# Kernel optimization log

Hardware: AMD Instinct MI355X
Metric: run time of the kernel (lower is better)

Reference implementation:

```python
import jax, jax.numpy as jnp
import numpy as np

MARGIN = 0.2  # TripletMarginLoss margin and TripletMarginMiner margin


def setup_inputs() -> dict:
    key = jax.random.key(0)
    k1, k2 = jax.random.split(key)
    embeddings = jax.random.normal(k1, (384, 256), dtype=jnp.float32)
    labels = jax.random.randint(k2, (384,), 0, 32)
    return {"embeddings": embeddings, "labels": labels}


def _pairwise_l2(e):
    # Euclidean distance matrix with sqrt-safe gradient at zero.
    sq = jnp.sum(e * e, axis=1)
    d2 = jnp.maximum(sq[:, None] + sq[None, :] - 2.0 * (e @ e.T), 0.0)
    pos = d2 > 0.0
    return jnp.sqrt(jnp.where(pos, d2, 1.0)) * pos


def reference(embeddings, labels):
    # pytorch-metric-learning LpDistance defaults: normalize_embeddings=True, p=2
    e = embeddings / jnp.maximum(
        jnp.linalg.norm(embeddings, axis=1, keepdims=True), 1e-12
    )
    D = _pairwise_l2(e)  # [B, B]
    n = D.shape[0]

    same = labels[:, None] == labels[None, :]
    eye = jnp.eye(n, dtype=bool)
    pos_mask = same & ~eye   # valid (anchor, positive) pairs
    neg_mask = ~same         # valid (anchor, negative) pairs

    ap = D[:, :, None]       # dist(anchor, positive), broadcast over negative
    an = D[:, None, :]       # dist(anchor, negative), broadcast over positive
    tm = an - ap             # miner's triplet_margin (is_inverted=False)

    valid = pos_mask[:, :, None] & neg_mask[:, None, :]     # [B, B, B]
    # semihard miner: 0 < an - ap <= margin
    semihard = valid & (tm > 0.0) & (tm <= MARGIN)

    # TripletMarginLoss per-triplet loss: relu(ap - an + margin) = relu(margin - tm)
    losses = jnp.where(semihard, jnp.maximum(MARGIN - tm, 0.0), 0.0)

    # AvgNonZeroReducer: mean over strictly-positive losses (0 if none)
    nz = jnp.sum(losses > 0.0)
    total = jnp.sum(losses)
    return jnp.where(nz > 0, total / jnp.maximum(nz, 1).astype(total.dtype), 0.0)
```

## Files before the change

kernel.cpp:

```cpp
#include <hip/hip_runtime.h>

#define N    384
#define DIM  256
#define MARGIN_F 0.2f


__global__ __launch_bounds__(DIM) void normalize_kernel(
    const float* __restrict__ emb, float* __restrict__ eT,
    float* __restrict__ sq, float* __restrict__ accum_sum,
    unsigned int* __restrict__ accum_cnt)
{
    const int row = blockIdx.x;
    const int tid = threadIdx.x;

    float v = emb[row * DIM + tid];
    float s = v * v;
    #pragma unroll
    for (int off = 32; off > 0; off >>= 1) s += __shfl_down(s, off, 64);
    __shared__ float wsum[4];
    const int wave = tid >> 6, lane = tid & 63;
    if (lane == 0) wsum[wave] = s;
    __syncthreads();
    if (tid == 0) wsum[0] = wsum[0] + wsum[1] + wsum[2] + wsum[3];
    __syncthreads();
    const float tot = wsum[0];

    const float inv = 1.0f / fmaxf(sqrtf(tot), 1e-12f);
    const float vn  = v * inv;
    eT[tid * N + row] = vn;

    if (tid == 0) {
        sq[row] = tot * inv * inv;
        if (row == 0) { accum_sum[0] = 0.0f; accum_cnt[0] = 0u; }
    }
}

__global__ __launch_bounds__(N) void dist_kernel(
    const float* __restrict__ eT, const float* __restrict__ sq,
    float* __restrict__ D)
{
    const int i = blockIdx.x;
    const int j = threadIdx.x;

    __shared__ float ei[DIM];
    if (j < DIM) ei[j] = eT[j * N + i];
    __syncthreads();

    float acc = 0.0f;
    #pragma unroll 8
    for (int k = 0; k < DIM; ++k)
        acc += ei[k] * eT[k * N + j];

    const float d2 = fmaxf(sq[i] + sq[j] - 2.0f * acc, 0.0f);
    D[i * N + j] = (d2 > 0.0f) ? sqrtf(d2) : 0.0f;
}

__global__ __launch_bounds__(256) void triplet_kernel(
    const float* __restrict__ D, const int* __restrict__ labels,
    float* __restrict__ accum_sum, unsigned int* __restrict__ accum_cnt)
{
    const int i   = blockIdx.x;
    const int tid = threadIdx.x;

    __shared__ float Drow[N];
    __shared__ int   lab[N];
    __shared__ int   posList[N];
    __shared__ int   nPos;
    if (tid == 0) nPos = 0;
    __syncthreads();

    for (int j = tid; j < N; j += 256) {
        Drow[j] = D[i * N + j];
        lab[j]  = labels[j];
    }
    __syncthreads();

    const int li = lab[i];
    for (int j = tid; j < N; j += 256) {
        if (lab[j] == li && j != i) {
            int idx = atomicAdd(&nPos, 1);
            posList[idx] = j;
        }
    }
    __syncthreads();

    float        lsum = 0.0f;
    unsigned int lcnt = 0u;
    const int np = nPos;
    for (int p = 0; p < np; ++p) {
        const float dj = Drow[posList[p]];
        for (int k = tid; k < N; k += 256) {
            if (lab[k] != li) {
                const float tm = Drow[k] - dj;
                if (tm > 0.0f && tm <= MARGIN_F) {
                    const float l = MARGIN_F - tm;
                    lsum += l;
                    if (l > 0.0f) lcnt++;
                }
            }
        }
    }

    #pragma unroll
    for (int off = 32; off > 0; off >>= 1) {
        lsum += __shfl_down(lsum, off, 64);
        lcnt += __shfl_down(lcnt, off, 64);
    }
    __shared__ float        sredS[4];
    __shared__ unsigned int sredC[4];
    const int wave = tid >> 6, lane = tid & 63;
    if (lane == 0) { sredS[wave] = lsum; sredC[wave] = lcnt; }
    __syncthreads();
    if (tid == 0) {
        const float        S = sredS[0] + sredS[1] + sredS[2] + sredS[3];
        const unsigned int C = sredC[0] + sredC[1] + sredC[2] + sredC[3];
        if (S != 0.0f || C != 0u) {
            atomicAdd(accum_sum, S);
            atomicAdd(accum_cnt, C);
        }
    }
}

__global__ void finalize_kernel(const float* __restrict__ accum_sum,
                                const unsigned int* __restrict__ accum_cnt,
                                float* __restrict__ out)
{
    const unsigned int c = accum_cnt[0];
    out[0] = (c > 0u) ? (accum_sum[0] / (float)c) : 0.0f;
}

extern "C" void kernel_launch(void* const* d_in, const int* in_sizes, int n_in,
                              void* d_out, int out_size, void* d_ws, size_t ws_size,
                              hipStream_t stream) {
    const float* emb    = (const float*)d_in[0];
    const int*   labels = (const int*)d_in[1];
    float*       out    = (float*)d_out;

    float* ws = (float*)d_ws;
    float* eT  = ws;
    float* sq  = eT + (size_t)DIM * N;
    float* Dm  = sq + N;
    float* accum_sum = Dm + (size_t)N * N;
    unsigned int* accum_cnt = (unsigned int*)(accum_sum + 1);

    normalize_kernel<<<N, DIM, 0, stream>>>(emb, eT, sq, accum_sum, accum_cnt);
    dist_kernel<<<N, N, 0, stream>>>(eT, sq, Dm);
    triplet_kernel<<<N, 256, 0, stream>>>(Dm, labels, accum_sum, accum_cnt);
    finalize_kernel<<<1, 1, 0, stream>>>(accum_sum, accum_cnt, out);
}
```

Baseline: 79.60 us.

## Fuse distance, triplet mining and finalize into one kernel with two anchors per block

Merges the distance, triplet and finalize kernels into one kernel where each block handles two anchor rows. Each block computes its distance rows straight into shared memory, so the full distance matrix is no longer written to and read back from global memory. Each eT column load is now reused for two anchors. A last-block-done counter writes the final mean, which removes the finalize launch. Only 192 blocks are launched, which may leave parts of the GPU idle, and the positive-loop work per thread is now set by the number of positives.

```diff
diff --git a/kernel.cpp b/kernel.cpp
--- a/kernel.cpp
+++ b/kernel.cpp
@@ -1,14 +1,17 @@
 #include <hip/hip_runtime.h>
 
-#define N    384
-#define DIM  256
+#define N        384
+#define DIM      256
 #define MARGIN_F 0.2f
+#define NANCH    2
+#define NBLK     (N / NANCH)
 
 
 __global__ __launch_bounds__(DIM) void normalize_kernel(
     const float* __restrict__ emb, float* __restrict__ eT,
-    float* __restrict__ sq, float* __restrict__ accum_sum,
-    unsigned int* __restrict__ accum_cnt)
+    float* __restrict__ sq, float* __restrict__ invn,
+    float* __restrict__ accum_sum, unsigned int* __restrict__ accum_cnt,
+    unsigned int* __restrict__ done_cnt)
 {
     const int row = blockIdx.x;
     const int tid = threadIdx.x;
@@ -26,72 +29,79 @@
     const float tot = wsum[0];
 
     const float inv = 1.0f / fmaxf(sqrtf(tot), 1e-12f);
-    const float vn  = v * inv;
-    eT[tid * N + row] = vn;
+    eT[tid * N + row] = v * inv;
 
     if (tid == 0) {
-        sq[row] = tot * inv * inv;
-        if (row == 0) { accum_sum[0] = 0.0f; accum_cnt[0] = 0u; }
+        sq[row]   = tot * inv * inv;
+        invn[row] = inv;
+        if (row == 0) { accum_sum[0] = 0.0f; accum_cnt[0] = 0u; done_cnt[0] = 0u; }
     }
 }
 
-__global__ __launch_bounds__(N) void dist_kernel(
-    const float* __restrict__ eT, const float* __restrict__ sq,
-    float* __restrict__ D)
+__global__ __launch_bounds__(N) void fused_kernel(
+    const float* __restrict__ emb, const float* __restrict__ eT,
+    const float* __restrict__ sq, const float* __restrict__ invn,
+    const int* __restrict__ labels,
+    float* __restrict__ accum_sum, unsigned int* __restrict__ accum_cnt,
+    unsigned int* __restrict__ done_cnt, float* __restrict__ out)
 {
-    const int i = blockIdx.x;
-    const int j = threadIdx.x;
+    const int i0  = blockIdx.x * NANCH;
+    const int tid = threadIdx.x;
 
-    __shared__ float ei[DIM];
-    if (j < DIM) ei[j] = eT[j * N + i];
+    __shared__ float ei[NANCH][DIM];
+    __shared__ float Drow[NANCH][N];
+    __shared__ int   lab[N];
+    __shared__ int   posList[NANCH][N];
+    __shared__ int   posCnt[NANCH];
+    __shared__ float sredS[N / 64];
+    __shared__ unsigned int sredC[N / 64];
+
+    for (int t = tid; t < NANCH * DIM; t += N) {
+        const int a = t >> 8, k = t & (DIM - 1);
+        ei[a][k] = emb[(i0 + a) * DIM + k] * invn[i0 + a];
+    }
+    lab[tid] = labels[tid];
+    if (tid < NANCH) posCnt[tid] = 0;
     __syncthreads();
 
-    float acc = 0.0f;
+    float acc0 = 0.0f, acc1 = 0.0f;
+    const float* __restrict__ col = eT + tid;
     #pragma unroll 8
-    for (int k = 0; k < DIM; ++k)
-        acc += ei[k] * eT[k * N + j];
-
-    const float d2 = fmaxf(sq[i] + sq[j] - 2.0f * acc, 0.0f);
-    D[i * N + j] = (d2 > 0.0f) ? sqrtf(d2) : 0.0f;
-}
-
-__global__ __launch_bounds__(256) void triplet_kernel(
-    const float* __restrict__ D, const int* __restrict__ labels,
-    float* __restrict__ accum_sum, unsigned int* __restrict__ accum_cnt)
-{
-    const int i   = blockIdx.x;
-    const int tid = threadIdx.x;
-
-    __shared__ float Drow[N];
-    __shared__ int   lab[N];
-    __shared__ int   posList[N];
-    __shared__ int   nPos;
-    if (tid == 0) nPos = 0;
-    __syncthreads();
-
-    for (int j = tid; j < N; j += 256) {
-        Drow[j] = D[i * N + j];
-        lab[j]  = labels[j];
+    for (int k = 0; k < DIM; ++k) {
+        const float ek = col[k * N];
+        acc0 += ei[0][k] * ek;
+        acc1 += ei[1][k] * ek;
+    }
+    const float sqj = sq[tid];
+    {
+        const float d2 = fmaxf(sq[i0] + sqj - 2.0f * acc0, 0.0f);
+        Drow[0][tid] = (d2 > 0.0f) ? sqrtf(d2) : 0.0f;
+    }
+    {
+        const float d2 = fmaxf(sq[i0 + 1] + sqj - 2.0f * acc1, 0.0f);
+        Drow[1][tid] = (d2 > 0.0f) ? sqrtf(d2) : 0.0f;
     }
     __syncthreads();
 
-    const int li = lab[i];
-    for (int j = tid; j < N; j += 256) {
-        if (lab[j] == li && j != i) {
-            int idx = atomicAdd(&nPos, 1);
-            posList[idx] = j;
-        }
+    const int lj = lab[tid];
+    #pragma unroll
+    for (int a = 0; a < NANCH; ++a) {
+        const int ia = i0 + a;
+        if (lj == lab[ia] && tid != ia)
+            posList[a][atomicAdd(&posCnt[a], 1)] = tid;
     }
     __syncthreads();
 
     float        lsum = 0.0f;
     unsigned int lcnt = 0u;
-    const int np = nPos;
-    for (int p = 0; p < np; ++p) {
-        const float dj = Drow[posList[p]];
-        for (int k = tid; k < N; k += 256) {
-            if (lab[k] != li) {
-                const float tm = Drow[k] - dj;
+    #pragma unroll
+    for (int a = 0; a < NANCH; ++a) {
+        const int   li = lab[i0 + a];
+        const float dk = Drow[a][tid];
+        if (lj != li) {
+            const int np = posCnt[a];
+            for (int p = 0; p < np; ++p) {
+                const float tm = dk - Drow[a][posList[a][p]];
                 if (tm > 0.0f && tm <= MARGIN_F) {
                     const float l = MARGIN_F - tm;
                     lsum += l;
@@ -106,27 +116,27 @@
         lsum += __shfl_down(lsum, off, 64);
         lcnt += __shfl_down(lcnt, off, 64);
     }
-    __shared__ float        sredS[4];
-    __shared__ unsigned int sredC[4];
     const int wave = tid >> 6, lane = tid & 63;
     if (lane == 0) { sredS[wave] = lsum; sredC[wave] = lcnt; }
     __syncthreads();
+
     if (tid == 0) {
-        const float        S = sredS[0] + sredS[1] + sredS[2] + sredS[3];
-        const unsigned int C = sredC[0] + sredC[1] + sredC[2] + sredC[3];
+        float        S = 0.0f;
+        unsigned int C = 0u;
+        #pragma unroll
+        for (int w = 0; w < N / 64; ++w) { S += sredS[w]; C += sredC[w]; }
         if (S != 0.0f || C != 0u) {
             atomicAdd(accum_sum, S);
             atomicAdd(accum_cnt, C);
         }
+        __threadfence();
+        const unsigned int prev = atomicAdd(done_cnt, 1);
+        if (prev == NBLK - 1) {
+            const float        Sall = atomicAdd(accum_sum, 0.0f);
+            const unsigned int Call = atomicAdd(accum_cnt, 0u);
+            out[0] = (Call > 0u) ? (Sall / (float)Call) : 0.0f;
+        }
     }
-}
-
-__global__ void finalize_kernel(const float* __restrict__ accum_sum,
-                                const unsigned int* __restrict__ accum_cnt,
-                                float* __restrict__ out)
-{
-    const unsigned int c = accum_cnt[0];
-    out[0] = (c > 0u) ? (accum_sum[0] / (float)c) : 0.0f;
 }
 
 extern "C" void kernel_launch(void* const* d_in, const int* in_sizes, int n_in,
@@ -136,15 +146,16 @@
     const int*   labels = (const int*)d_in[1];
     float*       out    = (float*)d_out;
 
-    float* ws = (float*)d_ws;
-    float* eT  = ws;
-    float* sq  = eT + (size_t)DIM * N;
-    float* Dm  = sq + N;
-    float* accum_sum = Dm + (size_t)N * N;
+    float* ws   = (float*)d_ws;
+    float* eT   = ws;
+    float* sq   = eT + (size_t)DIM * N;
+    float* invn = sq + N;
+    float* accum_sum = invn + N;
     unsigned int* accum_cnt = (unsigned int*)(accum_sum + 1);
+    unsigned int* done_cnt  = accum_cnt + 1;
 
-    normalize_kernel<<<N, DIM, 0, stream>>>(emb, eT, sq, accum_sum, accum_cnt);
-    dist_kernel<<<N, N, 0, stream>>>(eT, sq, Dm);
-    triplet_kernel<<<N, 256, 0, stream>>>(Dm, labels, accum_sum, accum_cnt);
-    finalize_kernel<<<1, 1, 0, stream>>>(accum_sum, accum_cnt, out);
+    normalize_kernel<<<N, DIM, 0, stream>>>(emb, eT, sq, invn,
+                                            accum_sum, accum_cnt, done_cnt);
+    fused_kernel<<<NBLK, N, 0, stream>>>(emb, eT, sq, invn, labels,
+                                         accum_sum, accum_cnt, done_cnt, out);
 }
```

After: 78.53 us. Within noise of the previous version (-1.3%).
